# Optimization experiments

Measured on AMD Instinct MI355X. Metric: run time of the kernel, lower is better.

Reference implementation:

```python
import jax, jax.numpy as jnp
import numpy as np

C, H, W = 512, 192, 192  # feature map dims; 3x3 patches at stride 3 (non-overlapping)


def setup_inputs() -> dict:
    key = jax.random.key(0)
    k1, k2 = jax.random.split(key)
    model_resp = jax.random.normal(k1, (1, C, H, W), dtype=jnp.float32)
    style_resp = jax.random.normal(k2, (1, C, H, W), dtype=jnp.float32)
    return {"model_resp": model_resp, "style_resp": style_resp}


def _unfold3(x):
    # torch.nn.Unfold(kernel=3, stride=3) on (1, C, H, W) -> (C*9, L) after the
    # module's view(patch_count, patch_size) (note: rows are feature channels,
    # columns are spatial locations, matching the original code's dim order).
    _, c, h, w = x.shape
    p = x[0].reshape(c, h // 3, 3, w // 3, 3)          # (c, ph, kh, pw, kw)
    p = p.transpose(0, 2, 4, 1, 3)                      # (c, kh, kw, ph, pw)
    return p.reshape(c * 9, (h // 3) * (w // 3))        # (A, L)


def reference(model_resp, style_resp):
    img = _unfold3(model_resp)                          # (A, L)
    sty = _unfold3(style_resp)                          # (A, L)
    img_norm = 1.0 / jnp.linalg.norm(img, axis=1)       # (A,)
    sty_norm = 1.0 / jnp.linalg.norm(sty, axis=1)       # (A,)
    S = img @ sty.T                                     # (A, A), S[i,j] = img_i . sty_j
    # Faithful to torch: expand(A, A) of a 1-D tensor broadcasts along dim 0,
    # i.e. multiplies COLUMNS by the normalizer vector.
    S1 = S * img_norm[None, :]
    S2 = S1.T * sty_norm[None, :]                       # S2[i,j] = img_norm[i]*sty_norm[j]*(img_j . sty_i)
    nearest = jnp.argmax(S2, axis=0)                    # (A,) int
    max_sim = jnp.max(S2, axis=0)                       # (A,) float (the online-max values)
    return nearest, max_sim
```

## Files before the change

kernel.cpp:

```cpp
#include <hip/hip_runtime.h>
#include <hip/hip_bf16.h>
#include <hip/hip_fp16.h>

#define A_DIM 4608
#define L_DIM 4096
#define CH    512
#define H_DIM 192
#define W_DIM 192

typedef _Float16 half8 __attribute__((ext_vector_type(8)));
typedef float   floatx4 __attribute__((ext_vector_type(4)));

__global__ __launch_bounds__(256) void prep_kernel(
    const float* __restrict__ x,
    _Float16* __restrict__ Uhi,
    _Float16* __restrict__ Ulo,
    float* __restrict__ nrecip) {
  const int a = blockIdx.x;
  const int c = a / 9, k = a % 9;
  const int kh = k / 3, kw = k % 3;
  const float* xc = x + (size_t)c * (H_DIM * W_DIM) + kh * W_DIM + kw;
  const int t = threadIdx.x;
  float ss = 0.f;
#pragma unroll
  for (int it = 0; it < 16; ++it) {
    const int l = it * 256 + t;
    const int ph = l >> 6, pw = l & 63;
    const float v = xc[(3 * ph) * W_DIM + 3 * pw];
    ss += v * v;
    const _Float16 hi = (_Float16)v;
    const _Float16 lo = (_Float16)(v - (float)hi);
    Uhi[(size_t)a * L_DIM + l] = hi;
    Ulo[(size_t)a * L_DIM + l] = lo;
  }
#pragma unroll
  for (int off = 32; off > 0; off >>= 1) ss += __shfl_down(ss, off, 64);
  __shared__ float wss[4];
  const int wid = t >> 6, lane = t & 63;
  if (lane == 0) wss[wid] = ss;
  __syncthreads();
  if (t == 0) {
    const float tot = wss[0] + wss[1] + wss[2] + wss[3];
    nrecip[a] = 1.0f / sqrtf(tot);
  }
}

#define GLDS(g, l)                                                          \
  __builtin_amdgcn_global_load_lds(                                        \
      (const __attribute__((address_space(1))) void*)(g),                   \
      (__attribute__((address_space(3))) void*)(l), 16, 0, 0)

__global__ __launch_bounds__(256) void gemm_max_kernel(
    const _Float16* __restrict__ Shi, const _Float16* __restrict__ Slo,
    const _Float16* __restrict__ Ihi, const _Float16* __restrict__ Ilo,
    const float* __restrict__ img_nr,
    unsigned long long* __restrict__ packed) {
  __shared__ _Float16 sAh[128 * 32];
  __shared__ _Float16 sAl[128 * 32];
  __shared__ _Float16 sBh[128 * 32];
  __shared__ _Float16 sBl[128 * 32];

  const int t = threadIdx.x;
  const int lane = t & 63, wv = t >> 6;
  const int wr = wv >> 1, wc = wv & 1;
  const int row0 = blockIdx.y * 128;
  const int col0 = blockIdx.x * 128;
  const int quad = lane >> 4;
  const int l15 = lane & 15;

  floatx4 acc[4][4];
#pragma unroll
  for (int rf = 0; rf < 4; ++rf)
#pragma unroll
    for (int cf = 0; cf < 4; ++cf) acc[rf][cf] = (floatx4)0.f;

  const int sr = t >> 2, sseg = t & 3;
  const size_t gA = (size_t)(row0 + sr) * L_DIM + sseg * 8;
  const size_t gB = (size_t)(col0 + sr) * L_DIM + sseg * 8;
  const int lofs = sr * 32 + sseg * 8;
  const size_t rskip = (size_t)64 * L_DIM;

  for (int k0 = 0; k0 < L_DIM; k0 += 32) {
    __syncthreads();
    GLDS(Shi + gA + k0,         &sAh[lofs]);
    GLDS(Shi + gA + k0 + rskip, &sAh[lofs + 2048]);
    GLDS(Slo + gA + k0,         &sAl[lofs]);
    GLDS(Slo + gA + k0 + rskip, &sAl[lofs + 2048]);
    GLDS(Ihi + gB + k0,         &sBh[lofs]);
    GLDS(Ihi + gB + k0 + rskip, &sBh[lofs + 2048]);
    GLDS(Ilo + gB + k0,         &sBl[lofs]);
    GLDS(Ilo + gB + k0 + rskip, &sBl[lofs + 2048]);
    __syncthreads();

    half8 ah[4], al[4], bh[4], bl[4];
#pragma unroll
    for (int rf = 0; rf < 4; ++rf) {
      const int off = (wr * 64 + rf * 16 + l15) * 32 + quad * 8;
      ah[rf] = *(const half8*)&sAh[off];
      al[rf] = *(const half8*)&sAl[off];
    }
#pragma unroll
    for (int cf = 0; cf < 4; ++cf) {
      const int off = (wc * 64 + cf * 16 + l15) * 32 + quad * 8;
      bh[cf] = *(const half8*)&sBh[off];
      bl[cf] = *(const half8*)&sBl[off];
    }
#pragma unroll
    for (int rf = 0; rf < 4; ++rf)
#pragma unroll
      for (int cf = 0; cf < 4; ++cf) {
        acc[rf][cf] = __builtin_amdgcn_mfma_f32_16x16x32_f16(ah[rf], bh[cf], acc[rf][cf], 0, 0, 0);
        acc[rf][cf] = __builtin_amdgcn_mfma_f32_16x16x32_f16(ah[rf], bl[cf], acc[rf][cf], 0, 0, 0);
        acc[rf][cf] = __builtin_amdgcn_mfma_f32_16x16x32_f16(al[rf], bh[cf], acc[rf][cf], 0, 0, 0);
      }
  }

  float nr[4][4];
#pragma unroll
  for (int rf = 0; rf < 4; ++rf) {
    const int i = row0 + wr * 64 + rf * 16 + quad * 4;
    const floatx4 n4 = *(const floatx4*)&img_nr[i];
#pragma unroll
    for (int r = 0; r < 4; ++r) nr[rf][r] = n4[r];
  }
#pragma unroll
  for (int cf = 0; cf < 4; ++cf) {
    const int j = col0 + wc * 64 + cf * 16 + l15;
    float best = -3.4e38f;
    int bi = 0x7FFFFFFF;
#pragma unroll
    for (int rf = 0; rf < 4; ++rf)
#pragma unroll
      for (int r = 0; r < 4; ++r) {
        const int i = row0 + wr * 64 + rf * 16 + quad * 4 + r;
        const float v = acc[rf][cf][r] * nr[rf][r];
        if (v > best) { best = v; bi = i; }
      }
#pragma unroll
    for (int off = 16; off < 64; off <<= 1) {
      const float ov = __shfl_xor(best, off, 64);
      const int oi = __shfl_xor(bi, off, 64);
      if (ov > best || (ov == best && oi < bi)) { best = ov; bi = oi; }
    }
    if (quad == 0) {
      const unsigned u = __float_as_uint(best);
      const unsigned key = (u & 0x80000000u) ? ~u : (u | 0x80000000u);
      const unsigned long long pk =
          ((unsigned long long)key << 32) | (unsigned)(~(unsigned)bi);
      atomicMax(&packed[j], pk);
    }
  }
}

__global__ __launch_bounds__(256) void finalize_kernel(
    const unsigned long long* __restrict__ packed,
    const float* __restrict__ sty_nr, float* __restrict__ out) {
  const int j = blockIdx.x * 256 + threadIdx.x;
  if (j >= A_DIM) return;
  const unsigned long long p = packed[j];
  const unsigned key = (unsigned)(p >> 32);
  const unsigned u = (key & 0x80000000u) ? (key ^ 0x80000000u) : ~key;
  const float v = __uint_as_float(u);
  const int idx = (int)(~(unsigned)(p & 0xFFFFFFFFu));
  out[j] = (float)idx;
  out[A_DIM + j] = v * sty_nr[j];
}

extern "C" void kernel_launch(void* const* d_in, const int* in_sizes, int n_in,
                              void* d_out, int out_size, void* d_ws, size_t ws_size,
                              hipStream_t stream) {
  const float* model = (const float*)d_in[0];
  const float* style = (const float*)d_in[1];
  float* out = (float*)d_out;
  char* ws = (char*)d_ws;

  const size_t usz = (size_t)A_DIM * L_DIM * 2;
  _Float16* img_hi = (_Float16*)(ws);
  _Float16* img_lo = (_Float16*)(ws + usz);
  _Float16* sty_hi = (_Float16*)(ws + 2 * usz);
  _Float16* sty_lo = (_Float16*)(ws + 3 * usz);
  float* img_nr = (float*)(ws + 4 * usz);
  float* sty_nr = img_nr + A_DIM;
  unsigned long long* packed = (unsigned long long*)(img_nr + 2 * A_DIM);

  hipMemsetAsync(packed, 0, (size_t)A_DIM * 8, stream);
  prep_kernel<<<A_DIM, 256, 0, stream>>>(model, img_hi, img_lo, img_nr);
  prep_kernel<<<A_DIM, 256, 0, stream>>>(style, sty_hi, sty_lo, sty_nr);
  gemm_max_kernel<<<dim3(36, 36), 256, 0, stream>>>(sty_hi, sty_lo, img_hi,
                                                    img_lo, img_nr, packed);
  finalize_kernel<<<18, 256, 0, stream>>>(packed, sty_nr, out);
}
```

Baseline: 782.1 us.

## Merge prep launches with 3-wide reads; reorder LDS tile to fragment-major layout

The two prep launches become one grid over (channel, kh, tensor). Each thread reads three adjacent kw values per patch row, so the strided global loads are better utilised and the launch count drops. In the GEMM, the LDS staging is remapped so each wave's 16-row fragment is stored contiguously in lane order. The half8 fragment reads then become linear per-lane accesses that avoid LDS bank conflicts. The risk is that the global-load-to-LDS pattern now touches rows in a less coalesced order per wave.

```diff
diff --git a/kernel.cpp b/kernel.cpp
--- a/kernel.cpp
+++ b/kernel.cpp
@@ -12,36 +12,51 @@
 typedef float   floatx4 __attribute__((ext_vector_type(4)));
 
 __global__ __launch_bounds__(256) void prep_kernel(
-    const float* __restrict__ x,
-    _Float16* __restrict__ Uhi,
-    _Float16* __restrict__ Ulo,
-    float* __restrict__ nrecip) {
-  const int a = blockIdx.x;
-  const int c = a / 9, k = a % 9;
-  const int kh = k / 3, kw = k % 3;
-  const float* xc = x + (size_t)c * (H_DIM * W_DIM) + kh * W_DIM + kw;
+    const float* __restrict__ x0, const float* __restrict__ x1,
+    _Float16* __restrict__ Uhi0, _Float16* __restrict__ Ulo0,
+    _Float16* __restrict__ Uhi1, _Float16* __restrict__ Ulo1,
+    float* __restrict__ nr0, float* __restrict__ nr1) {
+  const int which = blockIdx.z;
+  const float* __restrict__ x = which ? x1 : x0;
+  _Float16* __restrict__ Uhi = which ? Uhi1 : Uhi0;
+  _Float16* __restrict__ Ulo = which ? Ulo1 : Ulo0;
+  float* __restrict__ nrecip = which ? nr1 : nr0;
+
+  const int c = blockIdx.x, kh = blockIdx.y;
+  const int a0 = c * 9 + kh * 3;
+  const float* __restrict__ xb = x + (size_t)c * (H_DIM * W_DIM) + kh * W_DIM;
   const int t = threadIdx.x;
-  float ss = 0.f;
+
+  float ss0 = 0.f, ss1 = 0.f, ss2 = 0.f;
 #pragma unroll
   for (int it = 0; it < 16; ++it) {
     const int l = it * 256 + t;
     const int ph = l >> 6, pw = l & 63;
-    const float v = xc[(3 * ph) * W_DIM + 3 * pw];
-    ss += v * v;
-    const _Float16 hi = (_Float16)v;
-    const _Float16 lo = (_Float16)(v - (float)hi);
-    Uhi[(size_t)a * L_DIM + l] = hi;
-    Ulo[(size_t)a * L_DIM + l] = lo;
-  }
-#pragma unroll
-  for (int off = 32; off > 0; off >>= 1) ss += __shfl_down(ss, off, 64);
-  __shared__ float wss[4];
+    const float* __restrict__ p = xb + (3 * ph) * W_DIM + 3 * pw;
+    const float v0 = p[0], v1 = p[1], v2 = p[2];
+    ss0 += v0 * v0; ss1 += v1 * v1; ss2 += v2 * v2;
+    const _Float16 h0 = (_Float16)v0, h1 = (_Float16)v1, h2 = (_Float16)v2;
+    Uhi[(size_t)(a0 + 0) * L_DIM + l] = h0;
+    Uhi[(size_t)(a0 + 1) * L_DIM + l] = h1;
+    Uhi[(size_t)(a0 + 2) * L_DIM + l] = h2;
+    Ulo[(size_t)(a0 + 0) * L_DIM + l] = (_Float16)(v0 - (float)h0);
+    Ulo[(size_t)(a0 + 1) * L_DIM + l] = (_Float16)(v1 - (float)h1);
+    Ulo[(size_t)(a0 + 2) * L_DIM + l] = (_Float16)(v2 - (float)h2);
+  }
+  __shared__ float wss[3][4];
   const int wid = t >> 6, lane = t & 63;
-  if (lane == 0) wss[wid] = ss;
+  float s[3] = {ss0, ss1, ss2};
+#pragma unroll
+  for (int kw = 0; kw < 3; ++kw) {
+    float v = s[kw];
+#pragma unroll
+    for (int off = 32; off > 0; off >>= 1) v += __shfl_down(v, off, 64);
+    if (lane == 0) wss[kw][wid] = v;
+  }
   __syncthreads();
-  if (t == 0) {
-    const float tot = wss[0] + wss[1] + wss[2] + wss[3];
-    nrecip[a] = 1.0f / sqrtf(tot);
+  if (t < 3) {
+    const float tot = wss[t][0] + wss[t][1] + wss[t][2] + wss[t][3];
+    nrecip[a0 + t] = 1.0f / sqrtf(tot);
   }
 }
 
@@ -74,10 +89,11 @@
 #pragma unroll
     for (int cf = 0; cf < 4; ++cf) acc[rf][cf] = (floatx4)0.f;
 
-  const int sr = t >> 2, sseg = t & 3;
+  const int sr = ((t >> 6) << 4) | (t & 15);
+  const int sseg = (t >> 4) & 3;
   const size_t gA = (size_t)(row0 + sr) * L_DIM + sseg * 8;
   const size_t gB = (size_t)(col0 + sr) * L_DIM + sseg * 8;
-  const int lofs = sr * 32 + sseg * 8;
+  const int lofs = t * 8;
   const size_t rskip = (size_t)64 * L_DIM;
 
   for (int k0 = 0; k0 < L_DIM; k0 += 32) {
@@ -95,13 +111,13 @@
     half8 ah[4], al[4], bh[4], bl[4];
 #pragma unroll
     for (int rf = 0; rf < 4; ++rf) {
-      const int off = (wr * 64 + rf * 16 + l15) * 32 + quad * 8;
+      const int off = (wr * 4 + rf) * 512 + lane * 8;
       ah[rf] = *(const half8*)&sAh[off];
       al[rf] = *(const half8*)&sAl[off];
     }
 #pragma unroll
     for (int cf = 0; cf < 4; ++cf) {
-      const int off = (wc * 64 + cf * 16 + l15) * 32 + quad * 8;
+      const int off = (wc * 4 + cf) * 512 + lane * 8;
       bh[cf] = *(const half8*)&sBh[off];
       bl[cf] = *(const half8*)&sBl[off];
     }
@@ -184,8 +200,8 @@
   unsigned long long* packed = (unsigned long long*)(img_nr + 2 * A_DIM);
 
   hipMemsetAsync(packed, 0, (size_t)A_DIM * 8, stream);
-  prep_kernel<<<A_DIM, 256, 0, stream>>>(model, img_hi, img_lo, img_nr);
-  prep_kernel<<<A_DIM, 256, 0, stream>>>(style, sty_hi, sty_lo, sty_nr);
+  prep_kernel<<<dim3(CH, 3, 2), 256, 0, stream>>>(
+      model, style, img_hi, img_lo, sty_hi, sty_lo, img_nr, sty_nr);
   gemm_max_kernel<<<dim3(36, 36), 256, 0, stream>>>(sty_hi, sty_lo, img_hi,
                                                     img_lo, img_nr, packed);
   finalize_kernel<<<18, 256, 0, stream>>>(packed, sty_nr, out);
```

Measured after the change: 889.1 us. 1.14x slower.
